# Optimization experiments

Hardware: AMD Instinct MI355X
Metric: run time of the kernel (lower is better)

## Reference

```python
import jax, jax.numpy as jnp
import numpy as np

DIM = 2048
N_HEADS = 16
HEAD_DIM = 128
KV_HEADS = 1
ROPE_BASE = 10000.0


def _rope_tables(T, dim, dtype):
    inv_freq = 1.0 / (ROPE_BASE ** (jnp.arange(0, dim, 2, dtype=jnp.float32) / dim))
    t = jnp.arange(T, dtype=jnp.float32)
    freqs = jnp.einsum('i,j->ij', t, inv_freq)          # [T, dim/2]
    emb = jnp.concatenate([freqs, freqs], axis=-1)      # [T, dim]
    cos = jnp.cos(emb)[None, None, :, :].astype(dtype)  # [1,1,T,dim]
    sin = jnp.sin(emb)[None, None, :, :].astype(dtype)
    return cos, sin


def _rotate_half(x):
    x1, x2 = jnp.split(x, 2, axis=-1)
    return jnp.concatenate([-x2, x1], axis=-1)


def setup_inputs() -> dict:
    key = jax.random.key(0)
    k1, k2, k3, k4, k5 = jax.random.split(key, 5)
    B, T = 2, 2048
    x = jax.random.normal(k1, (B, T, DIM), dtype=jnp.float32)
    # additive causal mask: 0 on/below diagonal, -1e9 above
    causal = jnp.triu(jnp.full((T, T), -1e9, dtype=jnp.float32), k=1)
    attn_mask = causal[None, None, :, :]
    s = 1.0 / np.sqrt(DIM)
    wq = jax.random.normal(k2, (DIM, N_HEADS * HEAD_DIM), dtype=jnp.float32) * s
    wk = jax.random.normal(k3, (DIM, KV_HEADS * HEAD_DIM), dtype=jnp.float32) * s
    wv = jax.random.normal(k4, (DIM, KV_HEADS * HEAD_DIM), dtype=jnp.float32) * s
    wo = jax.random.normal(k5, (N_HEADS * HEAD_DIM, DIM), dtype=jnp.float32) * s
    return {"x": x, "attn_mask": attn_mask, "wq": wq, "wk": wk, "wv": wv, "wo": wo}


def reference(x, attn_mask, wq, wk, wv, wo):
    B, T, C = x.shape
    q = (x @ wq).reshape(B, T, N_HEADS, HEAD_DIM).transpose(0, 2, 1, 3)   # [B,H,T,d]
    k = (x @ wk).reshape(B, T, KV_HEADS, HEAD_DIM).transpose(0, 2, 1, 3)  # [B,1,T,d]
    v = (x @ wv).reshape(B, T, KV_HEADS, HEAD_DIM).transpose(0, 2, 1, 3)  # [B,1,T,d]
    cos, sin = _rope_tables(T, HEAD_DIM, x.dtype)
    q = q * cos + _rotate_half(q) * sin
    k = k * cos + _rotate_half(k) * sin
    # KV head broadcasts over the H dim inside matmul (MQA expand path)
    att = jnp.matmul(q, k.swapaxes(-1, -2)) / np.sqrt(HEAD_DIM)          # [B,H,T,T]
    att = att + attn_mask
    w = jax.nn.softmax(att, axis=-1)
    y = jnp.matmul(w, v)                                                  # [B,H,T,d]
    y = y.transpose(0, 2, 1, 3).reshape(B, T, N_HEADS * HEAD_DIM)
    y = y @ wo
    k_exp = jnp.broadcast_to(k, (B, N_HEADS, T, HEAD_DIM))
    v_exp = jnp.broadcast_to(v, (B, N_HEADS, T, HEAD_DIM))
    return y, k_exp, v_exp
```

## Files before the change

### kernel.cpp

```cpp
#include <hip/hip_runtime.h>
#include <hip/hip_bf16.h>
#include <cstdint>
#include <cstddef>

#define B_SZ   2
#define T_SEQ  2048
#define C_DIM  2048
#define NH     16
#define HD     128

typedef __attribute__((ext_vector_type(8))) short s8v;
typedef __attribute__((ext_vector_type(4))) float f32x4;

typedef __attribute__((address_space(3))) char lds_char;
typedef __attribute__((address_space(1))) const char glob_char;

#define QSCALE 0.12751887f

__device__ __forceinline__ unsigned short f2bf(float f) {
    union { float f; uint32_t i; } v; v.f = f;
    uint32_t r = (v.i + 0x7FFFu + ((v.i >> 16) & 1u)) >> 16;
    return (unsigned short)r;
}

__device__ __forceinline__ unsigned short cvt1_bf16(float f) {
    unsigned int w;
    asm("v_cvt_pk_bf16_f32 %0, %1, %2" : "=v"(w) : "v"(f), "v"(f));
    return (unsigned short)w;
}

template <int CTRL>
__device__ __forceinline__ float dpp_ror_f(float x) {
    int t = __builtin_amdgcn_update_dpp(__float_as_int(x), __float_as_int(x),
                                        CTRL, 0xf, 0xf, false);
    return __int_as_float(t);
}
__device__ __forceinline__ float rowmax16(float v) {
    v = fmaxf(v, dpp_ror_f<0x121>(v));
    v = fmaxf(v, dpp_ror_f<0x122>(v));
    v = fmaxf(v, dpp_ror_f<0x124>(v));
    v = fmaxf(v, dpp_ror_f<0x128>(v));
    return v;
}

__global__ void k_f32_to_bf16(const float* __restrict__ in,
                              unsigned short* __restrict__ out, int n4) {
    int i = blockIdx.x * blockDim.x + threadIdx.x;
    int stride = gridDim.x * blockDim.x;
    for (; i < n4; i += stride) {
        float4 v = reinterpret_cast<const float4*>(in)[i];
        ushort4 o;
        o.x = f2bf(v.x); o.y = f2bf(v.y); o.z = f2bf(v.z); o.w = f2bf(v.w);
        reinterpret_cast<ushort4*>(out)[i] = o;
    }
}

__global__ void k_transp_bf16(const float* __restrict__ in,
                              unsigned short* __restrict__ out,
                              int R, int C, int ldo) {
    __shared__ unsigned short tile[64][66];
    int x0 = blockIdx.x * 64, y0 = blockIdx.y * 64;
    int tx = threadIdx.x, ty = threadIdx.y;
#pragma unroll
    for (int j = 0; j < 16; ++j) {
        int r = y0 + ty + j * 4;
        tile[ty + j * 4][tx] = f2bf(in[(size_t)r * C + x0 + tx]);
    }
    __syncthreads();
#pragma unroll
    for (int j = 0; j < 16; ++j) {
        int orow = x0 + ty + j * 4;
        out[(size_t)orow * ldo + y0 + tx] = tile[tx][ty + j * 4];
    }
}

__global__ void k_rope_tab(float* __restrict__ cosT, float* __restrict__ sinT,
                           float* __restrict__ cosT2, float* __restrict__ sinT2) {
    int idx = blockIdx.x * blockDim.x + threadIdx.x;
    if (idx >= T_SEQ * 64) return;
    int t = idx >> 6, i = idx & 63;
    float inv = powf(10000.0f, -(float)i / 64.0f);
    float ang = (float)t * inv;
    float c = cosf(ang), s = sinf(ang);
    cosT[idx] = c;  sinT[idx] = s;
    cosT2[i * T_SEQ + t] = c;  sinT2[i * T_SEQ + t] = s;
}

#define BM 128
#define BN 128
#define BK 64

__global__ __launch_bounds__(256) void k_gemm_bt(
        const unsigned short* __restrict__ A,
        const unsigned short* __restrict__ Bt,
        float* __restrict__ C, int M, int N, int K, int ldc, int gx) {
    __shared__ char smem[BM * BK * 2 + BN * BK * 2];
    char* As = smem;
    char* Bs = smem + BM * BK * 2;
    int tid = threadIdx.x, lane = tid & 63, wid = tid >> 6;
    int nwg = gridDim.x, cpx = nwg >> 3;
    int orig = blockIdx.x;
    int wg = (orig & 7) * cpx + (orig >> 3);
    int bx = wg % gx, by = wg / gx;
    int m0 = by * BM, n0 = bx * BN;
    int wr = wid >> 1, wc = wid & 1;

    f32x4 acc[4][4] = {};

    int srow = wid * 32 + (lane >> 3);
    int cp = lane & 7;

    for (int k0 = 0; k0 < K; k0 += BK) {
#pragma unroll
        for (int i = 0; i < 4; ++i) {
            int row = srow + i * 8;
            int c = cp ^ (row & 7);
            const unsigned short* ga = A + (size_t)(m0 + row) * K + k0 + c * 8;
            const unsigned short* gb = Bt + (size_t)(n0 + row) * K + k0 + c * 8;
            __builtin_amdgcn_global_load_lds((glob_char*)ga,
                (lds_char*)(As + wid * 4096 + i * 1024), 16, 0, 0);
            __builtin_amdgcn_global_load_lds((glob_char*)gb,
                (lds_char*)(Bs + wid * 4096 + i * 1024), 16, 0, 0);
        }
        __syncthreads();

#pragma unroll
        for (int kc = 0; kc < 2; ++kc) {
            s8v af[4], bfr[4];
#pragma unroll
            for (int mi = 0; mi < 4; ++mi) {
                int row = wr * 64 + mi * 16 + (lane & 15);
                int slot = (kc * 4 + (lane >> 4)) ^ (row & 7);
                af[mi] = *reinterpret_cast<const s8v*>(As + row * 128 + slot * 16);
            }
#pragma unroll
            for (int ni = 0; ni < 4; ++ni) {
                int row = wc * 64 + ni * 16 + (lane & 15);
                int slot = (kc * 4 + (lane >> 4)) ^ (row & 7);
                bfr[ni] = *reinterpret_cast<const s8v*>(Bs + row * 128 + slot * 16);
            }
#pragma unroll
            for (int mi = 0; mi < 4; ++mi)
#pragma unroll
                for (int ni = 0; ni < 4; ++ni)
                    acc[mi][ni] = __builtin_amdgcn_mfma_f32_16x16x32_bf16(
                        af[mi], bfr[ni], acc[mi][ni], 0, 0, 0);
        }
        __syncthreads();
    }

#pragma unroll
    for (int mi = 0; mi < 4; ++mi) {
        int row = m0 + wr * 64 + mi * 16 + ((lane >> 4) << 2);
#pragma unroll
        for (int ni = 0; ni < 4; ++ni) {
            int col = n0 + wc * 64 + ni * 16 + (lane & 15);
            float* cp2 = C + (size_t)row * ldc + col;
#pragma unroll
            for (int r = 0; r < 4; ++r)
                cp2[(size_t)r * ldc] = acc[mi][ni][r];
        }
    }
}

__global__ __launch_bounds__(256) void k_gemm_qkv(
        const unsigned short* __restrict__ A,
        const unsigned short* __restrict__ Bt,
        const float* __restrict__ cosT2,
        const float* __restrict__ sinT2,
        unsigned short* __restrict__ qB,
        float* __restrict__ qkvKV) {
    const int GX = 18, K = 2048;
    __shared__ char smem[BM * BK * 2 + BN * BK * 2];
    char* As = smem;
    char* Bs = smem + BM * BK * 2;
    int tid = threadIdx.x, lane = tid & 63, wid = tid >> 6;
    int nwg = gridDim.x, cpx = nwg >> 3;
    int orig = blockIdx.x;
    int wg = (orig & 7) * cpx + (orig >> 3);
    int bx = wg % GX, by = wg / GX;
    int m0 = by * BM, n0 = bx * BN;
    int l15 = lane & 15, l4 = lane >> 4;

    f32x4 acc[2][8] = {};

    int srow = wid * 32 + (lane >> 3);
    int cp = lane & 7;

    for (int k0 = 0; k0 < K; k0 += BK) {
#pragma unroll
        for (int i = 0; i < 4; ++i) {
            int row = srow + i * 8;
            int c = cp ^ (row & 7);
            const unsigned short* ga = A + (size_t)(m0 + row) * K + k0 + c * 8;
            const unsigned short* gb = Bt + (size_t)(n0 + row) * K + k0 + c * 8;
            __builtin_amdgcn_global_load_lds((glob_char*)ga,
                (lds_char*)(As + wid * 4096 + i * 1024), 16, 0, 0);
            __builtin_amdgcn_global_load_lds((glob_char*)gb,
                (lds_char*)(Bs + wid * 4096 + i * 1024), 16, 0, 0);
        }
        __syncthreads();

#pragma unroll
        for (int kc = 0; kc < 2; ++kc) {
            s8v af[2], bfr[8];
#pragma unroll
            for (int mi = 0; mi < 2; ++mi) {
                int row = wid * 32 + mi * 16 + l15;
                int slot = (kc * 4 + l4) ^ (row & 7);
                af[mi] = *reinterpret_cast<const s8v*>(As + row * 128 + slot * 16);
            }
#pragma unroll
            for (int ni = 0; ni < 8; ++ni) {
                int row = ni * 16 + l15;
                int slot = (kc * 4 + l4) ^ (row & 7);
                bfr[ni] = *reinterpret_cast<const s8v*>(Bs + row * 128 + slot * 16);
            }
#pragma unroll
            for (int mi = 0; mi < 2; ++mi)
#pragma unroll
                for (int ni = 0; ni < 8; ++ni)
                    acc[mi][ni] = __builtin_amdgcn_mfma_f32_16x16x32_bf16(
                        af[mi], bfr[ni], acc[mi][ni], 0, 0, 0);
        }
        __syncthreads();
    }

    if (bx < 16) {
        int b = m0 >> 11, h = bx;
#pragma unroll
        for (int mi = 0; mi < 2; ++mi) {
            int t0 = (m0 + wid * 32 + mi * 16 + l4 * 4) & (T_SEQ - 1);
#pragma unroll
            for (int nip = 0; nip < 4; ++nip) {
                int d = nip * 16 + l15;
                float4 c4 = *reinterpret_cast<const float4*>(cosT2 + (size_t)d * T_SEQ + t0);
                float4 s4 = *reinterpret_cast<const float4*>(sinT2 + (size_t)d * T_SEQ + t0);
#pragma unroll
                for (int r = 0; r < 4; ++r) {
                    float x1 = acc[mi][nip][r];
                    float x2 = acc[mi][nip + 4][r];
                    float cc = (&c4.x)[r], ss = (&s4.x)[r];
                    float o1 = (x1 * cc - x2 * ss) * QSCALE;
                    float o2 = (x2 * cc + x1 * ss) * QSCALE;
                    size_t qoff = ((size_t)(b * NH + h) * T_SEQ + t0 + r) * HD + d;
                    qB[qoff] = cvt1_bf16(o1);
                    qB[qoff + 64] = cvt1_bf16(o2);
                }
            }
        }
    } else {
        int colb = (bx - 16) * 128;
#pragma unroll
        for (int mi = 0; mi < 2; ++mi) {
            int row = m0 + wid * 32 + mi * 16 + l4 * 4;
#pragma unroll
            for (int ni = 0; ni < 8; ++ni) {
                int col = colb + ni * 16 + l15;
                float* cp2 = qkvKV + (size_t)row * 256 + col;
#pragma unroll
                for (int r = 0; r < 4; ++r)
                    cp2[(size_t)r * 256] = acc[mi][ni][r];
            }
        }
    }
}

__global__ void k_kv_transform(const float* __restrict__ qkvKV,
                               const float* __restrict__ cosT,
                               const float* __restrict__ sinT,
                               unsigned short* __restrict__ kB,
                               unsigned short* __restrict__ vT,
                               float* __restrict__ kexp,
                               float* __restrict__ vexp) {
    int bt = blockIdx.x;
    int b = bt >> 11, t = bt & 2047;
    int tid = threadIdx.x;
    const float* base = qkvKV + (size_t)bt * 256;

    if (tid < 64) {
        int d = tid;
        float c = cosT[t * 64 + d], s = sinT[t * 64 + d];
        float k1 = base[d], k2 = base[d + 64];
        float o1 = k1 * c - k2 * s;
        float o2 = k2 * c + k1 * s;
        size_t koff = ((size_t)b * T_SEQ + t) * HD + d;
        kB[koff] = f2bf(o1);
        kB[koff + 64] = f2bf(o2);
#pragma unroll
        for (int h = 0; h < NH; ++h) {
            size_t eoff = ((size_t)(b * NH + h) * T_SEQ + t) * HD + d;
            kexp[eoff] = o1;
            kexp[eoff + 64] = o2;
        }
    }
    if (tid >= 128) {
        int d = tid - 128;
        float v = base[128 + d];
        vT[((size_t)b * HD + d) * T_SEQ + t] = f2bf(v);
#pragma unroll
        for (int h = 0; h < NH; ++h)
            vexp[((size_t)(b * NH + h) * T_SEQ + t) * HD + d] = v;
    }
}

__global__ __launch_bounds__(256, 3) void k_flash_attn(
        const unsigned short* __restrict__ qB,
        const unsigned short* __restrict__ kB,
        const unsigned short* __restrict__ vT,
        unsigned short* __restrict__ yattn) {
    __shared__ char smem[53248];
    int tid = threadIdx.x, lane = tid & 63, wvid = tid >> 6;
    int l15 = lane & 15, l4 = lane >> 4;
    int blk = blockIdx.x;
    int bh = blk & 31;
    int b = bh >> 4, h = bh & 15;
    int g = blk >> 5;
    int a = g & 7, qq = g >> 3;
    int u = (qq == 0) ? (31 - a) : (qq == 1) ? (16 + a)
          : (qq == 2) ? (15 - a) : a;
    int qrow0 = u * 64 + wvid * 16;

    char* pbase = smem + 49152 + wvid * 1024;

    const unsigned short* kbB   = kB + (size_t)b * T_SEQ * HD;
    const unsigned short* vbase = vT + (size_t)b * HD * T_SEQ;

    const unsigned short* qbase =
        qB + ((size_t)(b * NH + h) * T_SEQ + qrow0) * HD;
    s8v aq[4];
#pragma unroll
    for (int kc = 0; kc < 4; ++kc)
        aq[kc] = *reinterpret_cast<const s8v*>(
            qbase + (size_t)l15 * HD + kc * 32 + l4 * 8);

    float m_r[4], l_r[4];
#pragma unroll
    for (int r = 0; r < 4; ++r) { m_r[r] = -3e38f; l_r[r] = 0.f; }
    f32x4 o[8] = {};

    int NT = 2 * u + 2;

    auto stage = [&](int buf, int t) {
        int kv0 = t * 32;
        char* kdst = smem + buf * 16384;
        char* vdst = smem + buf * 16384 + 8192;
#pragma unroll
        for (int j = 0; j < 2; ++j) {
            int n = j * 256 + tid;
            int row = n >> 4, ch = n & 15;
            const unsigned short* src =
                kbB + (size_t)(kv0 + row) * HD + (ch ^ (row & 7)) * 8;
            __builtin_amdgcn_global_load_lds((glob_char*)src,
                (lds_char*)(kdst + j * 4096 + wvid * 1024), 16, 0, 0);
        }
#pragma unroll
        for (int j = 0; j < 2; ++j) {
            int n = j * 256 + tid;
            int row = n >> 2, ch = n & 3;
            const unsigned short* src =
                vbase + (size_t)row * T_SEQ + kv0 + (ch ^ ((row >> 1) & 3)) * 8;
            __builtin_amdgcn_global_load_lds((glob_char*)src,
                (lds_char*)(vdst + j * 4096 + wvid * 1024), 16, 0, 0);
        }
    };

    stage(0, 0);
    stage(1, 1);
    asm volatile("s_waitcnt vmcnt(4)" ::: "memory");
    __builtin_amdgcn_s_barrier();
    __builtin_amdgcn_sched_barrier(0);

    int cur = 0;
    for (int t = 0; t < NT; ++t) {
        int nb = cur + 2; if (nb >= 3) nb -= 3;
        if (t + 2 < NT) stage(nb, t + 2);
        int kv0 = t * 32;
        const char* Kc = smem + cur * 16384;
        const char* Vc = smem + cur * 16384 + 8192;
        int act = (kv0 <= qrow0 + 15);

        if (act) {
            f32x4 sfr[2] = {};
            __builtin_amdgcn_s_setprio(1);
#pragma unroll
            for (int kc = 0; kc < 4; ++kc) {
                s8v kf[2];
#pragma unroll
                for (int n = 0; n < 2; ++n) {
                    int row = n * 16 + l15;
                    int byte = row * 256 +
                        ((kc * 64 + l4 * 16) ^ ((row & 7) << 4));
                    kf[n] = *reinterpret_cast<const s8v*>(Kc + byte);
                }
#pragma unroll
                for (int n = 0; n < 2; ++n)
                    sfr[n] = __builtin_amdgcn_mfma_f32_16x16x32_bf16(
                        aq[kc], kf[n], sfr[n], 0, 0, 0);
            }
            __builtin_amdgcn_s_setprio(0);

            if (kv0 + 31 > qrow0) {
#pragma unroll
                for (int n = 0; n < 2; ++n)
#pragma unroll
                    for (int r = 0; r < 4; ++r) {
                        int col = kv0 + n * 16 + l15;
                        int row = qrow0 + (l4 << 2) + r;
                        if (col > row) sfr[n][r] = -1e9f;
                    }
            }

            float pm[4];
#pragma unroll
            for (int r = 0; r < 4; ++r)
                pm[r] = rowmax16(fmaxf(sfr[0][r], sfr[1][r]));
            int ok = (pm[0] <= m_r[0] + 8.0f) & (pm[1] <= m_r[1] + 8.0f) &
                     (pm[2] <= m_r[2] + 8.0f) & (pm[3] <= m_r[3] + 8.0f);
            if (!__all(ok)) {
#pragma unroll
                for (int r = 0; r < 4; ++r) {
                    float mn = fmaxf(m_r[r], pm[r]);
                    float al = exp2f(m_r[r] - mn);
                    l_r[r] *= al;
#pragma unroll
                    for (int ds = 0; ds < 8; ++ds)
                        o[ds][r] *= al;
                    m_r[r] = mn;
                }
            }
#pragma unroll
            for (int n = 0; n < 2; ++n)
#pragma unroll
                for (int r = 0; r < 4; ++r) {
                    float p = exp2f(sfr[n][r] - m_r[r]);
                    sfr[n][r] = p;
                    l_r[r] += p;
                }

#pragma unroll
            for (int n = 0; n < 2; ++n)
#pragma unroll
                for (int r = 0; r < 4; ++r) {
                    int rowl = (l4 << 2) + r;
                    int byte = rowl * 64 +
                        (((n * 16 + l15) * 2) ^ (((rowl ^ (rowl >> 2)) & 3) << 4));
                    *reinterpret_cast<unsigned short*>(pbase + byte) =
                        cvt1_bf16(sfr[n][r]);
                }
        }
        asm volatile("s_waitcnt lgkmcnt(0)" ::: "memory");
        __builtin_amdgcn_sched_barrier(0);

        if (act) {
            __builtin_amdgcn_s_setprio(1);
            int rowl = l15;
            int byte = rowl * 64 +
                ((l4 * 16) ^ (((rowl ^ (rowl >> 2)) & 3) << 4));
            s8v pa = *reinterpret_cast<const s8v*>(pbase + byte);
#pragma unroll
            for (int ds = 0; ds < 8; ++ds) {
                int vrow = ds * 16 + l15;
                int vbyte = vrow * 64 + ((l4 * 16) ^ (((vrow >> 1) & 3) << 4));
                s8v bv = *reinterpret_cast<const s8v*>(Vc + vbyte);
                o[ds] = __builtin_amdgcn_mfma_f32_16x16x32_bf16(
                    pa, bv, o[ds], 0, 0, 0);
            }
            __builtin_amdgcn_s_setprio(0);
        }

        if (t + 2 < NT) {
            asm volatile("s_waitcnt vmcnt(4) lgkmcnt(0)" ::: "memory");
        } else {
            asm volatile("s_waitcnt vmcnt(0) lgkmcnt(0)" ::: "memory");
        }
        __builtin_amdgcn_s_barrier();
        __builtin_amdgcn_sched_barrier(0);
        cur = (cur == 2) ? 0 : cur + 1;
    }

    float inv[4];
#pragma unroll
    for (int r = 0; r < 4; ++r) {
        float lv = l_r[r];
#pragma unroll
        for (int off = 1; off < 16; off <<= 1)
            lv += __shfl_xor(lv, off);
        inv[r] = 1.0f / lv;
    }
#pragma unroll
    for (int ds = 0; ds < 8; ++ds)
#pragma unroll
        for (int r = 0; r < 4; ++r) {
            int row = qrow0 + (l4 << 2) + r;
            int col = h * HD + ds * 16 + l15;
            yattn[((size_t)b * T_SEQ + row) * C_DIM + col] =
                cvt1_bf16(o[ds][r] * inv[r]);
        }
}

extern "C" void kernel_launch(void* const* d_in, const int* in_sizes, int n_in,
                              void* d_out, int out_size, void* d_ws, size_t ws_size,
                              hipStream_t stream) {
    const float* x  = (const float*)d_in[0];
    const float* wq = (const float*)d_in[2];
    const float* wk = (const float*)d_in[3];
    const float* wv = (const float*)d_in[4];
    const float* wo = (const float*)d_in[5];

    char* ws = (char*)d_ws;
    size_t off = 0;
    auto alloc = [&](size_t bytes) -> void* {
        void* p = ws + off;
        off += (bytes + 255) & ~(size_t)255;
        return p;
    };
    unsigned short* xb    = (unsigned short*)alloc((size_t)4096 * 2048 * 2);
    unsigned short* wT    = (unsigned short*)alloc((size_t)2304 * 2048 * 2);
    unsigned short* woT   = (unsigned short*)alloc((size_t)2048 * 2048 * 2);
    float*          qkvKV = (float*)alloc((size_t)4096 * 256 * 4);
    float*          cosT  = (float*)alloc((size_t)2048 * 64 * 4);
    float*          sinT  = (float*)alloc((size_t)2048 * 64 * 4);
    float*          cosT2 = (float*)alloc((size_t)64 * 2048 * 4);
    float*          sinT2 = (float*)alloc((size_t)64 * 2048 * 4);
    unsigned short* qB    = (unsigned short*)alloc((size_t)2 * 16 * 2048 * 128 * 2);
    unsigned short* kB    = (unsigned short*)alloc((size_t)2 * 2048 * 128 * 2);
    unsigned short* vT    = (unsigned short*)alloc((size_t)2 * 128 * 2048 * 2);
    unsigned short* yattn = (unsigned short*)alloc((size_t)4096 * 2048 * 2);

    float* y_out = (float*)d_out;
    float* kexp  = y_out + (size_t)2 * 2048 * 2048;
    float* vexp  = kexp + (size_t)2 * 16 * 2048 * 128;

    dim3 tb(64, 4);
    k_f32_to_bf16<<<2048, 256, 0, stream>>>(x, xb, 4096 * 2048 / 4);
    k_transp_bf16<<<dim3(32, 32), tb, 0, stream>>>(wq, wT, 2048, 2048, 2048);
    k_transp_bf16<<<dim3(2, 32), tb, 0, stream>>>(wk, wT + (size_t)2048 * 2048, 2048, 128, 2048);
    k_transp_bf16<<<dim3(2, 32), tb, 0, stream>>>(wv, wT + (size_t)2176 * 2048, 2048, 128, 2048);
    k_transp_bf16<<<dim3(32, 32), tb, 0, stream>>>(wo, woT, 2048, 2048, 2048);
    k_rope_tab<<<512, 256, 0, stream>>>(cosT, sinT, cosT2, sinT2);

    k_gemm_qkv<<<576, 256, 0, stream>>>(xb, wT, cosT2, sinT2, qB, qkvKV);
    k_kv_transform<<<4096, 256, 0, stream>>>(qkvKV, cosT, sinT, kB, vT, kexp, vexp);
    k_flash_attn<<<1024, 256, 0, stream>>>(qB, kB, vT, yattn);
    k_gemm_bt<<<512, 256, 0, stream>>>(
        yattn, woT, y_out, 4096, 2048, 2048, 2048, 16);
}
```

Measured before the change: 249.1 us.

## Compute transposed S tile so P stays in registers, dropping the LDS round-trip

```diff
diff --git a/kernel.cpp b/kernel.cpp
--- a/kernel.cpp
+++ b/kernel.cpp
@@ -28,19 +28,10 @@
     asm("v_cvt_pk_bf16_f32 %0, %1, %2" : "=v"(w) : "v"(f), "v"(f));
     return (unsigned short)w;
 }
-
-template <int CTRL>
-__device__ __forceinline__ float dpp_ror_f(float x) {
-    int t = __builtin_amdgcn_update_dpp(__float_as_int(x), __float_as_int(x),
-                                        CTRL, 0xf, 0xf, false);
-    return __int_as_float(t);
-}
-__device__ __forceinline__ float rowmax16(float v) {
-    v = fmaxf(v, dpp_ror_f<0x121>(v));
-    v = fmaxf(v, dpp_ror_f<0x122>(v));
-    v = fmaxf(v, dpp_ror_f<0x124>(v));
-    v = fmaxf(v, dpp_ror_f<0x128>(v));
-    return v;
+__device__ __forceinline__ unsigned int cvt2_bf16(float a, float b) {
+    unsigned int w;
+    asm("v_cvt_pk_bf16_f32 %0, %1, %2" : "=v"(w) : "v"(a), "v"(b));
+    return w;
 }
 
 __global__ void k_f32_to_bf16(const float* __restrict__ in,
@@ -309,7 +300,7 @@
         const unsigned short* __restrict__ kB,
         const unsigned short* __restrict__ vT,
         unsigned short* __restrict__ yattn) {
-    __shared__ char smem[53248];
+    __shared__ char smem[49152];
     int tid = threadIdx.x, lane = tid & 63, wvid = tid >> 6;
     int l15 = lane & 15, l4 = lane >> 4;
     int blk = blockIdx.x;
@@ -321,8 +312,6 @@
           : (qq == 2) ? (15 - a) : a;
     int qrow0 = u * 64 + wvid * 16;
 
-    char* pbase = smem + 49152 + wvid * 1024;
-
     const unsigned short* kbB   = kB + (size_t)b * T_SEQ * HD;
     const unsigned short* vbase = vT + (size_t)b * HD * T_SEQ;
 
@@ -334,9 +323,7 @@
         aq[kc] = *reinterpret_cast<const s8v*>(
             qbase + (size_t)l15 * HD + kc * 32 + l4 * 8);
 
-    float m_r[4], l_r[4];
-#pragma unroll
-    for (int r = 0; r < 4; ++r) { m_r[r] = -3e38f; l_r[r] = 0.f; }
+    float m = -3e38f, l = 0.f;
     f32x4 o[8] = {};
 
     int NT = 2 * u + 2;
@@ -396,75 +383,72 @@
 #pragma unroll
                 for (int n = 0; n < 2; ++n)
                     sfr[n] = __builtin_amdgcn_mfma_f32_16x16x32_bf16(
-                        aq[kc], kf[n], sfr[n], 0, 0, 0);
+                        kf[n], aq[kc], sfr[n], 0, 0, 0);
             }
             __builtin_amdgcn_s_setprio(0);
 
             if (kv0 + 31 > qrow0) {
+                int qa = qrow0 + l15;
 #pragma unroll
                 for (int n = 0; n < 2; ++n)
 #pragma unroll
                     for (int r = 0; r < 4; ++r) {
-                        int col = kv0 + n * 16 + l15;
-                        int row = qrow0 + (l4 << 2) + r;
-                        if (col > row) sfr[n][r] = -1e9f;
+                        int kv = kv0 + n * 16 + l4 * 4 + r;
+                        if (kv > qa) sfr[n][r] = -1e9f;
                     }
             }
 
-            float pm[4];
-#pragma unroll
-            for (int r = 0; r < 4; ++r)
-                pm[r] = rowmax16(fmaxf(sfr[0][r], sfr[1][r]));
-            int ok = (pm[0] <= m_r[0] + 8.0f) & (pm[1] <= m_r[1] + 8.0f) &
-                     (pm[2] <= m_r[2] + 8.0f) & (pm[3] <= m_r[3] + 8.0f);
-            if (!__all(ok)) {
+            float pm = sfr[0][0];
+#pragma unroll
+            for (int r = 1; r < 4; ++r) pm = fmaxf(pm, sfr[0][r]);
+#pragma unroll
+            for (int r = 0; r < 4; ++r) pm = fmaxf(pm, sfr[1][r]);
+            pm = fmaxf(pm, __shfl_xor(pm, 16));
+            pm = fmaxf(pm, __shfl_xor(pm, 32));
+            if (!__all(pm <= m + 8.0f)) {
+                float mn = fmaxf(m, pm);
+                float al = exp2f(m - mn);
+                l *= al;
+#pragma unroll
+                for (int ds = 0; ds < 8; ++ds)
+#pragma unroll
+                    for (int r = 0; r < 4; ++r) o[ds][r] *= al;
+                m = mn;
+            }
+#pragma unroll
+            for (int n = 0; n < 2; ++n)
 #pragma unroll
                 for (int r = 0; r < 4; ++r) {
-                    float mn = fmaxf(m_r[r], pm[r]);
-                    float al = exp2f(m_r[r] - mn);
-                    l_r[r] *= al;
-#pragma unroll
-                    for (int ds = 0; ds < 8; ++ds)
-                        o[ds][r] *= al;
-                    m_r[r] = mn;
+                    float p = exp2f(sfr[n][r] - m);
+                    sfr[n][r] = p;
+                    l += p;
                 }
-            }
-#pragma unroll
-            for (int n = 0; n < 2; ++n)
-#pragma unroll
-                for (int r = 0; r < 4; ++r) {
-                    float p = exp2f(sfr[n][r] - m_r[r]);
-                    sfr[n][r] = p;
-                    l_r[r] += p;
-                }
-
-#pragma unroll
-            for (int n = 0; n < 2; ++n)
-#pragma unroll
-                for (int r = 0; r < 4; ++r) {
-                    int rowl = (l4 << 2) + r;
-                    int byte = rowl * 64 +
-                        (((n * 16 + l15) * 2) ^ (((rowl ^ (rowl >> 2)) & 3) << 4));
-                    *reinterpret_cast<unsigned short*>(pbase + byte) =
-                        cvt1_bf16(sfr[n][r]);
-                }
-        }
-        asm volatile("s_waitcnt lgkmcnt(0)" ::: "memory");
-        __builtin_amdgcn_sched_barrier(0);
-
-        if (act) {
+
+            unsigned int a0 = cvt2_bf16(sfr[0][0], sfr[0][1]);
+            unsigned int a1 = cvt2_bf16(sfr[0][2], sfr[0][3]);
+            unsigned int b0 = cvt2_bf16(sfr[1][0], sfr[1][1]);
+            unsigned int b1 = cvt2_bf16(sfr[1][2], sfr[1][3]);
+            int srcE = (lane & 15) | ((lane & 16) << 1);
+            int srcO = srcE + 16;
+            unsigned int ae0 = __shfl(a0, srcE), ae1 = __shfl(a1, srcE);
+            unsigned int be0 = __shfl(b0, srcE), be1 = __shfl(b1, srcE);
+            unsigned int ao0 = __shfl(a0, srcO), ao1 = __shfl(a1, srcO);
+            unsigned int bo0 = __shfl(b0, srcO), bo1 = __shfl(b1, srcO);
+            bool lo = (lane & 32) == 0;
+            union { unsigned int u[4]; s8v v; } pf;
+            pf.u[0] = lo ? ae0 : be0;
+            pf.u[1] = lo ? ae1 : be1;
+            pf.u[2] = lo ? ao0 : bo0;
+            pf.u[3] = lo ? ao1 : bo1;
+
             __builtin_amdgcn_s_setprio(1);
-            int rowl = l15;
-            int byte = rowl * 64 +
-                ((l4 * 16) ^ (((rowl ^ (rowl >> 2)) & 3) << 4));
-            s8v pa = *reinterpret_cast<const s8v*>(pbase + byte);
 #pragma unroll
             for (int ds = 0; ds < 8; ++ds) {
                 int vrow = ds * 16 + l15;
                 int vbyte = vrow * 64 + ((l4 * 16) ^ (((vrow >> 1) & 3) << 4));
                 s8v bv = *reinterpret_cast<const s8v*>(Vc + vbyte);
                 o[ds] = __builtin_amdgcn_mfma_f32_16x16x32_bf16(
-                    pa, bv, o[ds], 0, 0, 0);
+                    bv, pf.v, o[ds], 0, 0, 0);
             }
             __builtin_amdgcn_s_setprio(0);
         }
@@ -479,24 +463,17 @@
         cur = (cur == 2) ? 0 : cur + 1;
     }
 
-    float inv[4];
-#pragma unroll
-    for (int r = 0; r < 4; ++r) {
-        float lv = l_r[r];
-#pragma unroll
-        for (int off = 1; off < 16; off <<= 1)
-            lv += __shfl_xor(lv, off);
-        inv[r] = 1.0f / lv;
-    }
-#pragma unroll
-    for (int ds = 0; ds < 8; ++ds)
-#pragma unroll
-        for (int r = 0; r < 4; ++r) {
-            int row = qrow0 + (l4 << 2) + r;
-            int col = h * HD + ds * 16 + l15;
-            yattn[((size_t)b * T_SEQ + row) * C_DIM + col] =
-                cvt1_bf16(o[ds][r] * inv[r]);
-        }
+    l += __shfl_xor(l, 16);
+    l += __shfl_xor(l, 32);
+    float inv = 1.0f / l;
+    size_t rowoff = ((size_t)b * T_SEQ + qrow0 + l15) * C_DIM + h * HD;
+#pragma unroll
+    for (int ds = 0; ds < 8; ++ds) {
+        uint2 w;
+        w.x = cvt2_bf16(o[ds][0] * inv, o[ds][1] * inv);
+        w.y = cvt2_bf16(o[ds][2] * inv, o[ds][3] * inv);
+        *reinterpret_cast<uint2*>(yattn + rowoff + ds * 16 + l4 * 4) = w;
+    }
 }
 
 extern "C" void kernel_launch(void* const* d_in, const int* in_sizes, int n_in,
```

Result: faster. 242.4 us (-2.7%).
